# Optimization experiments

Measured on AMD Instinct MI355X. Metric: run time of the kernel, lower is better.

Reference implementation:

```python
import jax, jax.numpy as jnp
import numpy as np

DIM = 2048
NUM_HEADS = 8
HEAD_DIM = DIM // NUM_HEADS
BATCH = 16384
EPS = 1e-5


def setup_inputs() -> dict:
    key = jax.random.key(0)
    ks = jax.random.split(key, 10)
    s = 1.0 / np.sqrt(DIM)
    inp = {
        "x": jax.random.normal(ks[0], (BATCH, 1, DIM), dtype=jnp.float32),
        "w_q": jax.random.uniform(ks[1], (DIM, DIM), jnp.float32, -s, s),
        "b_q": jax.random.uniform(ks[2], (DIM,), jnp.float32, -s, s),
        "w_k": jax.random.uniform(ks[3], (DIM, DIM), jnp.float32, -s, s),
        "b_k": jax.random.uniform(ks[4], (DIM,), jnp.float32, -s, s),
        "w_v": jax.random.uniform(ks[5], (DIM, DIM), jnp.float32, -s, s),
        "b_v": jax.random.uniform(ks[6], (DIM,), jnp.float32, -s, s),
        "w_o": jax.random.uniform(ks[7], (DIM, DIM), jnp.float32, -s, s),
        "b_o": jax.random.uniform(ks[8], (DIM,), jnp.float32, -s, s),
        "ln_gamma": jnp.ones((DIM,), jnp.float32),
        "ln_beta": jnp.zeros((DIM,), jnp.float32),
    }
    return inp


def _layer_norm(x, gamma, beta):
    mean = jnp.mean(x, axis=-1, keepdims=True)
    var = jnp.mean(jnp.square(x - mean), axis=-1, keepdims=True)
    return (x - mean) * jax.lax.rsqrt(var + EPS) * gamma + beta


def reference(x, w_q, b_q, w_k, b_k, w_v, b_v, w_o, b_o, ln_gamma, ln_beta):
    # x: (B, 1, D). Dropout is identity (eval mode).
    residual = x
    h = _layer_norm(x, ln_gamma, ln_beta)
    q = h @ w_q.T + b_q  # (B, 1, D)
    k = h @ w_k.T + b_k
    v = h @ w_v.T + b_v
    B = x.shape[0]
    # (B, H, 1, hd)
    qh = q.reshape(B, 1, NUM_HEADS, HEAD_DIM).transpose(0, 2, 1, 3)
    kh = k.reshape(B, 1, NUM_HEADS, HEAD_DIM).transpose(0, 2, 1, 3)
    vh = v.reshape(B, 1, NUM_HEADS, HEAD_DIM).transpose(0, 2, 1, 3)
    scale = HEAD_DIM ** -0.5
    # (B, H, 1, 1); with seq_len=1 softmax is trivially 1, but keep the math faithful
    scores = jnp.einsum("bhqd,bhkd->bhqk", qh, kh) * scale
    probs = jax.nn.softmax(scores, axis=-1)
    attn = jnp.einsum("bhqk,bhkd->bhqd", probs, vh)  # (B, H, 1, hd)
    attn = attn.transpose(0, 2, 1, 3).reshape(B, 1, DIM)
    out = attn @ w_o.T + b_o
    out = out + residual
    return out[:, 0, :]  # squeeze seq dim -> (B, D)
```

## Files before the change

### kernel.cpp

```cpp
#include <hip/hip_runtime.h>
#include <hip/hip_bf16.h>
#include <cstdint>

#define D_MODEL 2048
#define N_BATCH 16384

typedef __attribute__((ext_vector_type(8))) __bf16 bf16x8;
typedef __attribute__((ext_vector_type(4))) float f32x4;

__device__ __forceinline__ unsigned short f2bf(float f) {
    unsigned int u = __builtin_bit_cast(unsigned int, f);
    u += 0x7fffu + ((u >> 16) & 1u);
    return (unsigned short)(u >> 16);
}

__global__ __launch_bounds__(256) void prep_kernel(
    const float* __restrict__ w_v, const float* __restrict__ w_o,
    const float* __restrict__ b_v, const float* __restrict__ b_o,
    unsigned short* __restrict__ wvT, unsigned short* __restrict__ woB,
    float* __restrict__ b_c)
{
    __shared__ float tile[32][33];
    const int b = blockIdx.x;
    const int t = threadIdx.x;
    if (b < 4096) {
        const int nb = 64;
        const int k0 = (b % nb) * 32;
        const int j0 = (b / nb) * 32;
        const int tx = t & 31, ty0 = t >> 5;
        #pragma unroll
        for (int i = 0; i < 32; i += 8) {
            int j = ty0 + i;
            tile[j][tx] = w_v[(long)(j0 + j) * D_MODEL + k0 + tx];
        }
        __syncthreads();
        #pragma unroll
        for (int i = 0; i < 32; i += 8) {
            int kk = ty0 + i;
            wvT[(long)(k0 + kk) * D_MODEL + j0 + tx] = f2bf(tile[tx][kk]);
        }
    } else if (b < 6144) {
        long i = ((long)(b - 4096) * 256 + t) * 8;
        const float4* in4 = reinterpret_cast<const float4*>(w_o + i);
        float4 a = in4[0], bb = in4[1];
        union { unsigned short u[8]; uint4 v; } o;
        o.u[0] = f2bf(a.x); o.u[1] = f2bf(a.y); o.u[2] = f2bf(a.z); o.u[3] = f2bf(a.w);
        o.u[4] = f2bf(bb.x); o.u[5] = f2bf(bb.y); o.u[6] = f2bf(bb.z); o.u[7] = f2bf(bb.w);
        *reinterpret_cast<uint4*>(woB + i) = o.v;
    } else {
        const int n = b - 6144;
        const float4* w4 = reinterpret_cast<const float4*>(w_o + (long)n * D_MODEL);
        const float4* v4 = reinterpret_cast<const float4*>(b_v);
        float4 a = w4[t], bb = w4[256 + t], va = v4[t], vb = v4[256 + t];
        float s = a.x*va.x + a.y*va.y + a.z*va.z + a.w*va.w
                + bb.x*vb.x + bb.y*vb.y + bb.z*vb.z + bb.w*vb.w;
        #pragma unroll
        for (int off = 32; off; off >>= 1) s += __shfl_xor(s, off);
        float* red = &tile[0][0];
        const int lane = t & 63, wid = t >> 6;
        if (lane == 0) red[wid] = s;
        __syncthreads();
        if (t == 0) b_c[n] = red[0] + red[1] + red[2] + red[3] + b_o[n];
    }
}

__global__ __launch_bounds__(256) void lnwc_kernel(
    const unsigned short* __restrict__ A, const unsigned short* __restrict__ B,
    unsigned short* __restrict__ C,
    const float* __restrict__ x, const float* __restrict__ gamma,
    const float* __restrict__ beta, unsigned short* __restrict__ h)
{
    __shared__ __align__(16) unsigned short Alds[128 * 32];
    __shared__ __align__(16) unsigned short Blds[128 * 32];
    const int t = threadIdx.x;

    if (blockIdx.x < 256) {
        const int K = D_MODEL, N = D_MODEL;
        int wg = blockIdx.x;
        wg = (wg & 7) * 32 + (wg >> 3);
        const int bm = wg >> 4, bn = wg & 15;

        const int lane = t & 63, wid = t >> 6;
        const int wr = wid >> 1, wc = wid & 1;

        f32x4 acc[4][4];
        #pragma unroll
        for (int i = 0; i < 4; i++)
            #pragma unroll
            for (int j = 0; j < 4; j++) acc[i][j] = (f32x4){0.f, 0.f, 0.f, 0.f};

        const long Abase = (long)bm * 128 * K;
        const long Bbase = (long)bn * 128 * K;
        const int ci0 = wid * 64 + lane;
        const int ci1 = 256 + ci0;
        const int r0 = ci0 >> 2, c0 = (ci0 & 3) * 8;
        const int r1 = ci1 >> 2, c1 = (ci1 & 3) * 8;

        const int arow = wr * 64 + (lane & 15);
        const int brow = wc * 64 + (lane & 15);
        const int koff = (lane >> 4) * 8;

        for (int k0 = 0; k0 < K; k0 += 32) {
            __builtin_amdgcn_global_load_lds(
                (const __attribute__((address_space(1))) void*)(A + Abase + (long)r0 * K + k0 + c0),
                (__attribute__((address_space(3))) void*)(Alds + wid * 512), 16, 0, 0);
            __builtin_amdgcn_global_load_lds(
                (const __attribute__((address_space(1))) void*)(A + Abase + (long)r1 * K + k0 + c1),
                (__attribute__((address_space(3))) void*)(Alds + 2048 + wid * 512), 16, 0, 0);
            __builtin_amdgcn_global_load_lds(
                (const __attribute__((address_space(1))) void*)(B + Bbase + (long)r0 * K + k0 + c0),
                (__attribute__((address_space(3))) void*)(Blds + wid * 512), 16, 0, 0);
            __builtin_amdgcn_global_load_lds(
                (const __attribute__((address_space(1))) void*)(B + Bbase + (long)r1 * K + k0 + c1),
                (__attribute__((address_space(3))) void*)(Blds + 2048 + wid * 512), 16, 0, 0);
            __syncthreads();

            bf16x8 af[4], bfr[4];
            #pragma unroll
            for (int m = 0; m < 4; m++)
                af[m] = *reinterpret_cast<const bf16x8*>(&Alds[(arow + m * 16) * 32 + koff]);
            #pragma unroll
            for (int n = 0; n < 4; n++)
                bfr[n] = *reinterpret_cast<const bf16x8*>(&Blds[(brow + n * 16) * 32 + koff]);
            #pragma unroll
            for (int m = 0; m < 4; m++)
                #pragma unroll
                for (int n = 0; n < 4; n++)
                    acc[m][n] = __builtin_amdgcn_mfma_f32_16x16x32_bf16(af[m], bfr[n], acc[m][n], 0, 0, 0);
            __syncthreads();
        }

        const int crow0 = bm * 128 + wr * 64 + ((lane >> 4) << 2);
        const int ccol0 = bn * 128 + wc * 64 + (lane & 15);
        #pragma unroll
        for (int m = 0; m < 4; m++)
            #pragma unroll
            for (int j = 0; j < 4; j++) {
                const long r = crow0 + m * 16 + j;
                #pragma unroll
                for (int n = 0; n < 4; n++)
                    C[r * N + ccol0 + n * 16] = f2bf(acc[m][n][j]);
            }
    } else {
        const int row = blockIdx.x - 256;
        const float4* x4 = reinterpret_cast<const float4*>(x + (long)row * D_MODEL);
        float4 a = x4[t];
        float4 b = x4[256 + t];
        float s  = a.x + a.y + a.z + a.w + b.x + b.y + b.z + b.w;
        float ss = a.x*a.x + a.y*a.y + a.z*a.z + a.w*a.w
                 + b.x*b.x + b.y*b.y + b.z*b.z + b.w*b.w;
        #pragma unroll
        for (int off = 32; off; off >>= 1) {
            s  += __shfl_xor(s, off);
            ss += __shfl_xor(ss, off);
        }
        float* red = reinterpret_cast<float*>(Alds);
        const int lane = t & 63, wid = t >> 6;
        if (lane == 0) { red[wid*2] = s; red[wid*2+1] = ss; }
        __syncthreads();
        s  = red[0] + red[2] + red[4] + red[6];
        ss = red[1] + red[3] + red[5] + red[7];
        const float mean = s * (1.0f / D_MODEL);
        const float var  = ss * (1.0f / D_MODEL) - mean * mean;
        const float inv  = rsqrtf(var + 1e-5f);

        const float4* g4  = reinterpret_cast<const float4*>(gamma);
        const float4* be4 = reinterpret_cast<const float4*>(beta);
        ushort4* h4 = reinterpret_cast<ushort4*>(h + (long)row * D_MODEL);
        {
            float4 g = g4[t], be = be4[t];
            ushort4 o;
            o.x = f2bf((a.x - mean) * inv * g.x + be.x);
            o.y = f2bf((a.y - mean) * inv * g.y + be.y);
            o.z = f2bf((a.z - mean) * inv * g.z + be.z);
            o.w = f2bf((a.w - mean) * inv * g.w + be.w);
            h4[t] = o;
        }
        {
            float4 g = g4[256 + t], be = be4[256 + t];
            ushort4 o;
            o.x = f2bf((b.x - mean) * inv * g.x + be.x);
            o.y = f2bf((b.y - mean) * inv * g.y + be.y);
            o.z = f2bf((b.z - mean) * inv * g.z + be.z);
            o.w = f2bf((b.w - mean) * inv * g.w + be.w);
            h4[256 + t] = o;
        }
    }
}

#define GLL(src, dst) __builtin_amdgcn_global_load_lds( \
    (const __attribute__((address_space(1))) void*)(src), \
    (__attribute__((address_space(3))) void*)(dst), 16, 0, 0)
#define WAITV4() do { asm volatile("s_waitcnt vmcnt(4)" ::: "memory"); \
                      __builtin_amdgcn_sched_barrier(0); } while (0)
#define WAITV0() do { asm volatile("s_waitcnt vmcnt(0)" ::: "memory"); \
                      __builtin_amdgcn_sched_barrier(0); } while (0)

__global__ __launch_bounds__(512, 2) void gemm_bt_8ph(
    const unsigned short* __restrict__ A, const unsigned short* __restrict__ B,
    float* __restrict__ C, const float* __restrict__ bias,
    const float* __restrict__ resid, int M, int N, int K)
{
    __shared__ __align__(16) char ldsb[131072];

    const int nBN = N >> 8;
    int wg = blockIdx.x;
    const int cpx = gridDim.x >> 3;
    wg = (wg & 7) * cpx + (wg >> 3);
    const int bm = wg / nBN, bn = wg % nBN;

    const int t = threadIdx.x;
    const int lane = t & 63, wid = t >> 6;
    const int wr = wid >> 2;
    const int wc = wid & 3;

    const long Kl = K;
    const int tr = t >> 3;
    const int c8 = ((t & 7) ^ (tr & 7)) * 8;
    const unsigned short* As = A + (long)(bm * 256 + tr) * Kl + c8;
    const unsigned short* Bs = B + (long)(bn * 256 + tr) * Kl + c8;

#define ST_A(buf, half, kcol) do { \
    const unsigned short* s_ = As + (half) * 128 * Kl + (kcol); \
    char* d_ = ldsb + (buf) * 65536 + (half) * 16384 + t * 16; \
    GLL(s_, d_); GLL(s_ + 64 * Kl, d_ + 8192); } while (0)
#define ST_B(buf, half, kcol) do { \
    const unsigned short* s_ = Bs + (half) * 128 * Kl + (kcol); \
    char* d_ = ldsb + (buf) * 65536 + 32768 + (half) * 16384 + t * 16; \
    GLL(s_, d_); GLL(s_ + 64 * Kl, d_ + 8192); } while (0)

    const int l15 = lane & 15, l4 = lane >> 4;
    const int swz0 = ((l4)     ^ (l15 & 7)) << 4;
    const int swz1 = ((4 + l4) ^ (l15 & 7)) << 4;
    const int aOff = wr * 16384 + l15 * 128;
    const int bOff = 32768 + (wc >> 1) * 16384 + ((wc & 1) * 64 + l15) * 128;

#define LDV(off) (*reinterpret_cast<const bf16x8*>(ldsb + (off)))
#define RD_A(buf, mh) do { \
    _Pragma("unroll") for (int mi = 0; mi < 4; ++mi) \
        af[mi][0] = LDV((buf) * 65536 + aOff + ((mh) * 4 + mi) * 2048 + swz0); \
    _Pragma("unroll") for (int mi = 0; mi < 4; ++mi) \
        af[mi][1] = LDV((buf) * 65536 + aOff + ((mh) * 4 + mi) * 2048 + swz1); } while (0)
#define RD_B0(buf) do { \
    _Pragma("unroll") for (int nj = 0; nj < 2; ++nj) \
        b0[nj][0] = LDV((buf) * 65536 + bOff + nj * 2048 + swz0); \
    _Pragma("unroll") for (int nj = 0; nj < 2; ++nj) \
        b0[nj][1] = LDV((buf) * 65536 + bOff + nj * 2048 + swz1); } while (0)
#define RD_B1(buf) do { \
    _Pragma("unroll") for (int nj = 0; nj < 2; ++nj) \
        b1[nj][0] = LDV((buf) * 65536 + bOff + (2 + nj) * 2048 + swz0); \
    _Pragma("unroll") for (int nj = 0; nj < 2; ++nj) \
        b1[nj][1] = LDV((buf) * 65536 + bOff + (2 + nj) * 2048 + swz1); } while (0)

#define MMQ(mh, nh, BQ) do { \
    __builtin_amdgcn_s_setprio(1); \
    _Pragma("unroll") for (int kk = 0; kk < 2; ++kk) \
    _Pragma("unroll") for (int mi = 0; mi < 4; ++mi) \
    _Pragma("unroll") for (int nj = 0; nj < 2; ++nj) \
        acc[(mh) * 4 + mi][(nh) * 2 + nj] = __builtin_amdgcn_mfma_f32_16x16x32_bf16( \
            af[mi][kk], BQ[nj][kk], acc[(mh) * 4 + mi][(nh) * 2 + nj], 0, 0, 0); \
    __builtin_amdgcn_s_setprio(0); } while (0)
#define ENDP() __builtin_amdgcn_s_barrier()

    bf16x8 af[4][2], b0[2][2], b1[2][2];
    f32x4 acc[8][4];
    #pragma unroll
    for (int i = 0; i < 8; i++)
        #pragma unroll
        for (int j = 0; j < 4; j++) acc[i][j] = (f32x4){0.f, 0.f, 0.f, 0.f};

    const int NI = K >> 7;

    ST_A(0, 0, 0); ST_A(0, 1, 0); ST_B(0, 0, 0); ST_B(0, 1, 0);
    ST_B(1, 0, 64); ST_A(1, 0, 64);
    WAITV4();
    __builtin_amdgcn_s_barrier();

    for (int i = 0; i < NI; ++i) {
        const int kcA1 = (i << 7) + 64;
        const int kcN0 = (i << 7) + 128;
        const int kcN1 = (i << 7) + 192;
        const bool more = (i + 1 < NI);

        RD_A(0, 0); RD_B0(0);
        ST_A(1, 1, kcA1);
        MMQ(0, 0, b0); ENDP();
        RD_B1(0);
        ST_B(1, 1, kcA1);
        MMQ(0, 1, b1); ENDP();
        RD_A(0, 1);
        if (more) ST_B(0, 0, kcN0);
        MMQ(1, 0, b0); ENDP();
        if (more) ST_A(0, 0, kcN0);
        MMQ(1, 1, b1);
        if (more) { WAITV4(); } else { WAITV0(); }
        ENDP();
        RD_A(1, 0); RD_B0(1);
        if (more) ST_A(0, 1, kcN0);
        MMQ(0, 0, b0); ENDP();
        RD_B1(1);
        if (more) ST_B(0, 1, kcN0);
        MMQ(0, 1, b1); ENDP();
        RD_A(1, 1);
        if (more) ST_B(1, 0, kcN1);
        MMQ(1, 0, b0); ENDP();
        if (more) ST_A(1, 0, kcN1);
        MMQ(1, 1, b1);
        if (more) { WAITV4(); }
        ENDP();
    }
#undef ST_A
#undef ST_B
#undef RD_A
#undef RD_B0
#undef RD_B1
#undef MMQ
#undef ENDP
#undef LDV

    float* ldsf = reinterpret_cast<float*>(ldsb);
    float bias4[4];
    #pragma unroll
    for (int n = 0; n < 4; n++)
        bias4[n] = bias[bn * 256 + wc * 64 + l15 + n * 16];
    const int wcol = wc * 64 + l15;

    #pragma unroll
    for (int rd = 0; rd < 4; ++rd) {
        __syncthreads();
        if (wr == (rd >> 1)) {
            #pragma unroll
            for (int mm = 0; mm < 4; ++mm) {
                const int m = (rd & 1) * 4 + mm;
                #pragma unroll
                for (int j = 0; j < 4; ++j) {
                    const int rl = mm * 16 + l4 * 4 + j;
                    #pragma unroll
                    for (int n = 0; n < 4; ++n)
                        ldsf[rl * 260 + wcol + n * 16] = acc[m][n][j] + bias4[n];
                }
            }
        }
        __syncthreads();
        const long gr0 = (long)bm * 256 + rd * 64;
        #pragma unroll
        for (int rr = 0; rr < 8; ++rr) {
            const int rl = wid * 8 + rr;
            const long go = (gr0 + rl) * N + bn * 256 + lane * 4;
            float4 v = *reinterpret_cast<const float4*>(&ldsf[rl * 260 + lane * 4]);
            const float4 rv = *reinterpret_cast<const float4*>(&resid[go]);
            v.x += rv.x; v.y += rv.y; v.z += rv.z; v.w += rv.w;
            *reinterpret_cast<float4*>(&C[go]) = v;
        }
    }
}

extern "C" void kernel_launch(void* const* d_in, const int* in_sizes, int n_in,
                              void* d_out, int out_size, void* d_ws, size_t ws_size,
                              hipStream_t stream) {
    const float* x     = (const float*)d_in[0];
    const float* w_v   = (const float*)d_in[5];
    const float* b_v   = (const float*)d_in[6];
    const float* w_o   = (const float*)d_in[7];
    const float* b_o   = (const float*)d_in[8];
    const float* gamma = (const float*)d_in[9];
    const float* beta  = (const float*)d_in[10];
    float* out = (float*)d_out;

    char* ws = (char*)d_ws;
    unsigned short* h   = (unsigned short*)(ws);
    unsigned short* wvT = (unsigned short*)(ws + 67108864L);
    unsigned short* woB = (unsigned short*)(ws + 67108864L + 8388608L);
    unsigned short* Wc  = (unsigned short*)(ws + 67108864L + 2 * 8388608L);
    float*          b_c = (float*)(ws + 67108864L + 3 * 8388608L);

    prep_kernel<<<8192, 256, 0, stream>>>(w_v, w_o, b_v, b_o, wvT, woB, b_c);
    lnwc_kernel<<<256 + N_BATCH, 256, 0, stream>>>(woB, wvT, Wc, x, gamma, beta, h);
    gemm_bt_8ph<<<(N_BATCH / 256) * (D_MODEL / 256), 512, 0, stream>>>(
        h, Wc, out, b_c, x, N_BATCH, D_MODEL, D_MODEL);
}
```

Before: 220.9 us.

## Merge GEMM main-loop phases into four larger phases with fewer barriers

Restructures the software-pipelined bf16 MFMA main loop from eight phases per iteration to four. Each phase now issues paired LDS reads, paired global-to-LDS stores and two MFMA quadrants before one barrier. The prologue and the stage assignment of the A/B buffer loads are reordered to match. The aim is to halve barrier count and give the scheduler bigger MFMA blocks to overlap with memory traffic. The cost is less interleaving of loads and MFMAs and higher register pressure, and the vmcnt wait counts must still match the new load ordering.

```diff
diff --git a/kernel.cpp b/kernel.cpp
--- a/kernel.cpp
+++ b/kernel.cpp
@@ -272,7 +272,7 @@
     const int NI = K >> 7;
 
     ST_A(0, 0, 0); ST_A(0, 1, 0); ST_B(0, 0, 0); ST_B(0, 1, 0);
-    ST_B(1, 0, 64); ST_A(1, 0, 64);
+    ST_B(1, 0, 64); ST_B(1, 1, 64);
     WAITV4();
     __builtin_amdgcn_s_barrier();
 
@@ -282,30 +282,20 @@
         const int kcN1 = (i << 7) + 192;
         const bool more = (i + 1 < NI);
 
-        RD_A(0, 0); RD_B0(0);
-        ST_A(1, 1, kcA1);
-        MMQ(0, 0, b0); ENDP();
-        RD_B1(0);
-        ST_B(1, 1, kcA1);
-        MMQ(0, 1, b1); ENDP();
+        RD_A(0, 0); RD_B0(0); RD_B1(0);
+        ST_A(1, 0, kcA1); ST_A(1, 1, kcA1);
+        MMQ(0, 0, b0); MMQ(0, 1, b1); ENDP();
         RD_A(0, 1);
-        if (more) ST_B(0, 0, kcN0);
-        MMQ(1, 0, b0); ENDP();
-        if (more) ST_A(0, 0, kcN0);
-        MMQ(1, 1, b1);
+        if (more) { ST_B(0, 0, kcN0); ST_B(0, 1, kcN0); }
+        MMQ(1, 0, b0); MMQ(1, 1, b1);
         if (more) { WAITV4(); } else { WAITV0(); }
         ENDP();
-        RD_A(1, 0); RD_B0(1);
-        if (more) ST_A(0, 1, kcN0);
-        MMQ(0, 0, b0); ENDP();
-        RD_B1(1);
-        if (more) ST_B(0, 1, kcN0);
-        MMQ(0, 1, b1); ENDP();
+        RD_A(1, 0); RD_B0(1); RD_B1(1);
+        if (more) { ST_A(0, 0, kcN0); ST_A(0, 1, kcN0); }
+        MMQ(0, 0, b0); MMQ(0, 1, b1); ENDP();
         RD_A(1, 1);
-        if (more) ST_B(1, 0, kcN1);
-        MMQ(1, 0, b0); ENDP();
-        if (more) ST_A(1, 0, kcN1);
-        MMQ(1, 1, b1);
+        if (more) { ST_B(1, 0, kcN1); ST_B(1, 1, kcN1); }
+        MMQ(1, 0, b0); MMQ(1, 1, b1);
         if (more) { WAITV4(); }
         ENDP();
     }
```

Result: no change. 223.3 us (+1.1%).
